# Performance work log

Measured on AMD Instinct MI355X. Metric: run time of the kernel, lower is better.

## Reference

```python
import jax, jax.numpy as jnp
import numpy as np

DIM = 4096
N_HEADS = 32
N_KV_HEADS = 8
HEAD_DIM = 128
ROPE_THETA = 10000.0
REPEATS = N_HEADS // N_KV_HEADS
SCALE = HEAD_DIM ** -0.5


def rope(x, seq_len, offset):
    # x: [b, h, seq_len, head_dim]; faithful to source: cos/sin from cat((freqs,freqs)),
    # rotate built by interleaved pair swap then flatten.
    d = x.shape[-1]
    inv_freq = 1.0 / (ROPE_THETA ** (jnp.arange(0, d, 2, dtype=jnp.float32) / d))  # [d/2]
    t = jnp.arange(offset, offset + seq_len, dtype=jnp.float32)                    # [L]
    freqs = t[:, None] * inv_freq[None, :]                                         # [L, d/2]
    emb = jnp.concatenate([freqs, freqs], axis=-1)                                 # [L, d]
    cos_emb = jnp.cos(emb)
    sin_emb = jnp.sin(emb)
    x_even = x[..., 0::2]
    x_odd = x[..., 1::2]
    rotate_x = jnp.stack([-x_odd, x_even], axis=-1).reshape(x.shape)
    return x * cos_emb + rotate_x * sin_emb


def setup_inputs() -> dict:
    key = jax.random.key(0)
    k1, k2, k3, k4, k5 = jax.random.split(key, 5)
    b, l = 1, 2048
    s = 0.02
    x = jax.random.normal(k1, (b, l, DIM), dtype=jnp.float32)
    wq = jax.random.normal(k2, (DIM, N_HEADS * HEAD_DIM), dtype=jnp.float32) * s
    wk = jax.random.normal(k3, (DIM, N_KV_HEADS * HEAD_DIM), dtype=jnp.float32) * s
    wv = jax.random.normal(k4, (DIM, N_KV_HEADS * HEAD_DIM), dtype=jnp.float32) * s
    wo = jax.random.normal(k5, (N_HEADS * HEAD_DIM, DIM), dtype=jnp.float32) * s
    return {"x": x, "wq": wq, "wk": wk, "wv": wv, "wo": wo, "seq_len": l}


def reference(x, wq, wk, wv, wo, seq_len):
    b, l, _ = x.shape
    q = (x @ wq).reshape(b, l, N_HEADS, HEAD_DIM).transpose(0, 2, 1, 3)       # [b,H,l,d]
    k = (x @ wk).reshape(b, l, N_KV_HEADS, HEAD_DIM).transpose(0, 2, 1, 3)    # [b,Hk,l,d]
    v = (x @ wv).reshape(b, l, N_KV_HEADS, HEAD_DIM).transpose(0, 2, 1, 3)
    # repeat KV heads to match query heads (GQA)
    k = jnp.repeat(k, REPEATS, axis=1)   # [b,H,l,d]
    v = jnp.repeat(v, REPEATS, axis=1)
    offset = 0  # cache is None
    q = rope(q, seq_len, offset)
    k = rope(k, seq_len, offset)
    scores = jnp.einsum('bhid,bhjd->bhij', q * SCALE, k)
    scores = jax.nn.softmax(scores.astype(jnp.float32), axis=-1).astype(scores.dtype)
    out = jnp.einsum('bhij,bhjd->bhid', scores, v)
    out = out.transpose(0, 2, 1, 3).reshape(b, l, N_HEADS * HEAD_DIM)
    return out @ wo, (k, v)
```

## Files before the change

### kernel.cpp

```cpp
#include <hip/hip_runtime.h>
#include <cstdint>
#include <cstddef>

#define DIM 4096
#define SEQ 2048
#define NH 32
#define NKV 8
#define HD 128
#define QKVN 6144

typedef __bf16 bf16_t;
typedef __bf16 bf16x8 __attribute__((ext_vector_type(8)));
typedef __bf16 bf16x4 __attribute__((ext_vector_type(4)));
typedef __bf16 bf16x2 __attribute__((ext_vector_type(2)));
typedef float f32x4 __attribute__((ext_vector_type(4)));
typedef int int4v __attribute__((ext_vector_type(4)));

__device__ __forceinline__ f32x4 mfma16(bf16x8 a, bf16x8 b, f32x4 c) {
  return __builtin_amdgcn_mfma_f32_16x16x32_bf16(a, b, c, 0, 0, 0);
}

__device__ __forceinline__ void async16(const bf16_t* g, bf16_t* l) {
  __builtin_amdgcn_global_load_lds((__attribute__((address_space(1))) void*)g,
                                   (__attribute__((address_space(3))) void*)l,
                                   16, 0, 0);
}

__device__ __forceinline__ int pack2(float a, float b) {
  bf16x2 h = { (bf16_t)a, (bf16_t)b };
  return __builtin_bit_cast(int, h);
}

#define LGKM0() do { asm volatile("s_waitcnt lgkmcnt(0)" ::: "memory"); \
                     __builtin_amdgcn_sched_barrier(0); } while (0)

template <int N> __device__ __forceinline__ void vmw() {
  if constexpr (N == 3) asm volatile("s_waitcnt vmcnt(3)" ::: "memory");
  else if constexpr (N == 4) asm volatile("s_waitcnt vmcnt(4)" ::: "memory");
  else if constexpr (N == 5) asm volatile("s_waitcnt vmcnt(5)" ::: "memory");
  else if constexpr (N == 6) asm volatile("s_waitcnt vmcnt(6)" ::: "memory");
  __builtin_amdgcn_sched_barrier(0);
}

__global__ void cast_x(const float* __restrict__ x, bf16_t* __restrict__ xb) {
  int i = blockIdx.x * 256 + threadIdx.x;
  const float4 v = ((const float4*)x)[i];
  bf16x4 o = { (bf16_t)v.x, (bf16_t)v.y, (bf16_t)v.z, (bf16_t)v.w };
  *(bf16x4*)(xb + (size_t)i * 4) = o;
}

__global__ void tcast(const float* __restrict__ src, bf16_t* __restrict__ dst,
                      int Ncols, int Kdim) {
  __shared__ float tile[32][33];
  int n0 = blockIdx.x * 32, k0 = blockIdx.y * 32;
  int tx = threadIdx.x, ty = threadIdx.y;
#pragma unroll
  for (int r = 0; r < 4; r++)
    tile[ty + 8 * r][tx] = src[(size_t)(k0 + ty + 8 * r) * Ncols + n0 + tx];
  __syncthreads();
#pragma unroll
  for (int r = 0; r < 4; r++)
    dst[(size_t)(n0 + ty + 8 * r) * Kdim + k0 + tx] = (bf16_t)tile[tx][ty + 8 * r];
}

template <int NF>
__global__ __launch_bounds__(512) void gemm256(const bf16_t* __restrict__ A,
                                               const bf16_t* __restrict__ Bt,
                                               float* __restrict__ C,
                                               int M, int N, int K) {
  constexpr int NA = NF - 1;
  constexpr int S1 = 2 + NA;
  __shared__ bf16_t As[2][16384];
  __shared__ bf16_t Bs[2][NF * 4096];
  const int t = threadIdx.x;
  const int lane = t & 63;
  const int l15 = lane & 15, quad = lane >> 4;
  const int w = t >> 6, wm = w >> 2, wn = w & 3;
  const int cgx = l15 & 7;

  const int gx = gridDim.x;
  const int nwg = gx * gridDim.y;
  const int id = blockIdx.y * gx + blockIdx.x;
  const int swz = (id & 7) * (nwg >> 3) + (id >> 3);
  const int bm = (swz / gx) * 256, bn = (swz % gx) * (NF * 64);

  const int srow = t >> 3;
  const int scol = ((t & 7) ^ (srow & 7)) << 3;
  const bf16_t* gA = A + (size_t)(bm + srow) * K + scol;
  const bf16_t* gB = Bt + (size_t)(bn + srow) * K + scol;
  const int ldst = t * 8;

  f32x4 acc[8][NF] = {};
  bf16x8 af[4][2], bfa[NA][2], bfb[2];

  auto sb1 = [&](int b2, int kk) {
    async16(gA + kk, &As[b2][ldst]);
    async16(gA + (size_t)64 * K + kk, &As[b2][4096 + ldst]);
    async16(gB + kk, &Bs[b2][ldst]);
    if constexpr (NF == 3) async16(gB + (size_t)64 * K + kk, &Bs[b2][4096 + ldst]);
  };
  auto sb2 = [&](int b2, int kk) {
    async16(gB + (size_t)((NF - 1) * 64) * K + kk, &Bs[b2][(NF - 1) * 4096 + ldst]);
  };
  auto sb3 = [&](int b2, int kk) {
    async16(gA + (size_t)128 * K + kk, &As[b2][8192 + ldst]);
    async16(gA + (size_t)192 * K + kk, &As[b2][12288 + ldst]);
  };

  sb1(0, 0);
  sb2(0, 0);
  sb3(0, 0);
  vmw<3>();
  __builtin_amdgcn_s_barrier();

  const int nkt = K >> 6;
  for (int kt = 0; kt < nkt; ++kt) {
    const int buf = kt & 1;
    const int k1 = (kt + 1) << 6;
    const bool pf = (kt + 1) < nkt;

#pragma unroll
    for (int mi = 0; mi < 4; mi++)
#pragma unroll
      for (int s = 0; s < 2; s++)
        af[mi][s] = *(const bf16x8*)&As[buf][(wm * 64 + mi * 16 + l15) * 64 +
                                            (((s << 2) | quad) ^ cgx) * 8];
#pragma unroll
    for (int ni = 0; ni < NA; ni++)
#pragma unroll
      for (int s = 0; s < 2; s++)
        bfa[ni][s] = *(const bf16x8*)&Bs[buf][(ni * 64 + wn * 16 + l15) * 64 +
                                              (((s << 2) | quad) ^ cgx) * 8];
    if (pf) sb1(buf ^ 1, k1);
    __builtin_amdgcn_s_barrier();
    LGKM0();
    __builtin_amdgcn_s_setprio(1);
#pragma unroll
    for (int mi = 0; mi < 4; mi++)
#pragma unroll
      for (int ni = 0; ni < NA; ni++)
#pragma unroll
        for (int s = 0; s < 2; s++)
          acc[mi][ni] = mfma16(af[mi][s], bfa[ni][s], acc[mi][ni]);
    __builtin_amdgcn_s_setprio(0);
    vmw<2 + S1>();
    __builtin_amdgcn_s_barrier();

#pragma unroll
    for (int s = 0; s < 2; s++)
      bfb[s] = *(const bf16x8*)&Bs[buf][((NF - 1) * 64 + wn * 16 + l15) * 64 +
                                        (((s << 2) | quad) ^ cgx) * 8];
    if (pf) sb2(buf ^ 1, k1);
    __builtin_amdgcn_s_barrier();
    LGKM0();
    __builtin_amdgcn_s_setprio(1);
#pragma unroll
    for (int mi = 0; mi < 4; mi++)
#pragma unroll
      for (int s = 0; s < 2; s++)
        acc[mi][NF - 1] = mfma16(af[mi][s], bfb[s], acc[mi][NF - 1]);
    __builtin_amdgcn_s_setprio(0);
    vmw<1 + S1>();
    __builtin_amdgcn_s_barrier();

#pragma unroll
    for (int mi = 0; mi < 4; mi++)
#pragma unroll
      for (int s = 0; s < 2; s++)
        af[mi][s] = *(const bf16x8*)&As[buf][(128 + wm * 64 + mi * 16 + l15) * 64 +
                                             (((s << 2) | quad) ^ cgx) * 8];
    if (pf) sb3(buf ^ 1, k1);
    __builtin_amdgcn_s_barrier();
    LGKM0();
    __builtin_amdgcn_s_setprio(1);
#pragma unroll
    for (int mi = 0; mi < 4; mi++)
#pragma unroll
      for (int s = 0; s < 2; s++)
        acc[mi + 4][NF - 1] = mfma16(af[mi][s], bfb[s], acc[mi + 4][NF - 1]);
    __builtin_amdgcn_s_setprio(0);
    __builtin_amdgcn_s_barrier();

#pragma unroll
    for (int ni = 0; ni < NA; ni++)
#pragma unroll
      for (int s = 0; s < 2; s++)
        bfa[ni][s] = *(const bf16x8*)&Bs[buf][(ni * 64 + wn * 16 + l15) * 64 +
                                              (((s << 2) | quad) ^ cgx) * 8];
    __builtin_amdgcn_s_barrier();
    LGKM0();
    __builtin_amdgcn_s_setprio(1);
#pragma unroll
    for (int mi = 0; mi < 4; mi++)
#pragma unroll
      for (int ni = 0; ni < NA; ni++)
#pragma unroll
        for (int s = 0; s < 2; s++)
          acc[mi + 4][ni] = mfma16(af[mi][s], bfa[ni][s], acc[mi + 4][ni]);
    __builtin_amdgcn_s_setprio(0);
    vmw<3>();
    __builtin_amdgcn_s_barrier();
  }

#pragma unroll
  for (int mi = 0; mi < 8; mi++)
#pragma unroll
    for (int ni = 0; ni < NF; ni++) {
      size_t row = (size_t)bm + (mi >> 2) * 128 + wm * 64 + (mi & 3) * 16 + quad * 4;
      size_t col = (size_t)bn + ni * 64 + wn * 16 + l15;
#pragma unroll
      for (int r = 0; r < 4; r++)
        C[(row + r) * N + col] = acc[mi][ni][r];
    }
}

__global__ void rope_scatter(const float* __restrict__ qkv, bf16_t* __restrict__ Qb,
                             bf16_t* __restrict__ Kb, bf16_t* __restrict__ Vt,
                             float* __restrict__ kOut, float* __restrict__ vOut) {
  int idx = blockIdx.x * 256 + threadIdx.x;
  int t = idx / 3072;
  int p = idx - t * 3072;
  const float NEG_L2T_64 = -0.20762050593046f;
  const float SS = 0.08838834764831845f * 1.4426950408889634f;
  if (p < 2048) {
    int hh = p >> 6, pr = p & 63;
    int d0 = pr << 1;
    const float* src = qkv + (size_t)t * QKVN + hh * HD + d0;
    float a = src[0], b = src[1];
    int j0 = d0 & 63, j1 = (d0 + 1) & 63;
    float th0 = (float)t * exp2f((float)j0 * NEG_L2T_64);
    float th1 = (float)t * exp2f((float)j1 * NEG_L2T_64);
    float o0 = (a * cosf(th0) - b * sinf(th0)) * SS;
    float o1 = (b * cosf(th1) + a * sinf(th1)) * SS;
    bf16_t* dst = Qb + ((size_t)hh * SEQ + t) * HD + d0;
    dst[0] = (bf16_t)o0;
    dst[1] = (bf16_t)o1;
  } else if (p < 2560) {
    int q2 = p - 2048;
    int kh = q2 >> 6, pr = q2 & 63;
    int d0 = pr << 1;
    const float* src = qkv + (size_t)t * QKVN + 4096 + kh * HD + d0;
    float a = src[0], b = src[1];
    int j0 = d0 & 63, j1 = (d0 + 1) & 63;
    float th0 = (float)t * exp2f((float)j0 * NEG_L2T_64);
    float th1 = (float)t * exp2f((float)j1 * NEG_L2T_64);
    float o0 = a * cosf(th0) - b * sinf(th0);
    float o1 = b * cosf(th1) + a * sinf(th1);
    bf16_t* dst = Kb + ((size_t)kh * SEQ + t) * HD + d0;
    dst[0] = (bf16_t)o0;
    dst[1] = (bf16_t)o1;
#pragma unroll
    for (int rep = 0; rep < 4; rep++) {
      float* kp = kOut + ((size_t)(kh * 4 + rep) * SEQ + t) * HD + d0;
      kp[0] = o0;
      kp[1] = o1;
    }
  } else {
    int q2 = p - 2560;
    int kh = q2 >> 6, pr = q2 & 63;
    int d0 = pr << 1;
    const float* src = qkv + (size_t)t * QKVN + 5120 + kh * HD + d0;
    float a = src[0], b = src[1];
#pragma unroll
    for (int rep = 0; rep < 4; rep++) {
      float* vp = vOut + ((size_t)(kh * 4 + rep) * SEQ + t) * HD + d0;
      vp[0] = a;
      vp[1] = b;
    }
    int tp = (t & ~31) + ((t & 12) << 1) + (t & 3) + ((t & 16) >> 2);
    Vt[((size_t)kh * HD + d0) * SEQ + tp] = (bf16_t)a;
    Vt[((size_t)kh * HD + d0 + 1) * SEQ + tp] = (bf16_t)b;
  }
}

__global__ __launch_bounds__(512, 2) void attn_kernel(const bf16_t* __restrict__ Qb,
                                                      const bf16_t* __restrict__ Kb,
                                                      const bf16_t* __restrict__ Vt,
                                                      bf16_t* __restrict__ AO) {
  __shared__ bf16_t Ks[2][8192];
  __shared__ bf16_t Vs[2][8192];
  const int h = blockIdx.y, kh = h >> 2;
  const int qbase = blockIdx.x * 256;
  const int w = threadIdx.x >> 6, lane = threadIdx.x & 63;
  const int l15 = lane & 15, quad = lane >> 4;
  const bf16_t* KbH = Kb + (size_t)kh * SEQ * HD;
  const bf16_t* VtH = Vt + (size_t)kh * HD * SEQ;

  bf16x8 qf[2][4];
#pragma unroll
  for (int nq = 0; nq < 2; nq++) {
    const bf16_t* qp = Qb + ((size_t)h * SEQ + qbase + w * 32 + nq * 16 + l15) * HD + quad * 8;
#pragma unroll
    for (int kc = 0; kc < 4; kc++) qf[nq][kc] = *(const bf16x8*)(qp + kc * 32);
  }

  f32x4 acc[8][2] = {};
  float rsum[2] = {0.f, 0.f};

  auto stage = [&](int buf, int kt0) {
    if (w < 4) {
      int kc = w;
#pragma unroll
      for (int kg = 0; kg < 4; kg++) {
        const bf16_t* g = KbH + (size_t)(kt0 + kg * 16 + (lane >> 2)) * HD + kc * 32 + (lane & 3) * 8;
        async16(g, &Ks[buf][kc * 2048 + kg * 512]);
      }
    } else {
      int vi = w - 4, kt = vi >> 1, dg0 = (vi & 1) * 4;
#pragma unroll
      for (int j = 0; j < 4; j++) {
        int dg = dg0 + j;
        const bf16_t* g = VtH + (size_t)(dg * 16 + (lane >> 2)) * SEQ + kt0 + kt * 32 + (lane & 3) * 8;
        async16(g, &Vs[buf][kt * 4096 + dg * 512]);
      }
    }
  };

  stage(0, 0);
  int buf = 0;

  for (int kt0 = 0; kt0 < SEQ; kt0 += 64, buf ^= 1) {
    __syncthreads();
    if (kt0 + 64 < SEQ) stage(buf ^ 1, kt0 + 64);

    f32x4 sacc[4][2] = {};
#pragma unroll
    for (int mi = 0; mi < 4; mi++)
#pragma unroll
      for (int kc = 0; kc < 4; kc++) {
        bf16x8 kf = *(const bf16x8*)(&Ks[buf][(kc * 64 + mi * 16 + l15) * 32 + quad * 8]);
#pragma unroll
        for (int nq = 0; nq < 2; nq++)
          sacc[mi][nq] = mfma16(kf, qf[nq][kc], sacc[mi][nq]);
      }

    int pk[4][2][2];
#pragma unroll
    for (int mi = 0; mi < 4; mi++)
#pragma unroll
      for (int nq = 0; nq < 2; nq++) {
        float p0 = exp2f(sacc[mi][nq][0]);
        float p1 = exp2f(sacc[mi][nq][1]);
        float p2 = exp2f(sacc[mi][nq][2]);
        float p3 = exp2f(sacc[mi][nq][3]);
        rsum[nq] += (p0 + p1) + (p2 + p3);
        pk[mi][nq][0] = pack2(p0, p1);
        pk[mi][nq][1] = pack2(p2, p3);
      }

#pragma unroll
    for (int kt = 0; kt < 2; kt++) {
#pragma unroll
      for (int nq = 0; nq < 2; nq++) {
        int4v dw;
        dw[0] = pk[2 * kt][nq][0];
        dw[1] = pk[2 * kt][nq][1];
        dw[2] = pk[2 * kt + 1][nq][0];
        dw[3] = pk[2 * kt + 1][nq][1];
        bf16x8 pf = __builtin_bit_cast(bf16x8, dw);
#pragma unroll
        for (int dt = 0; dt < 8; dt++) {
          bf16x8 vf = *(const bf16x8*)(&Vs[buf][(kt * 128 + dt * 16 + l15) * 32 + quad * 8]);
          acc[dt][nq] = mfma16(vf, pf, acc[dt][nq]);
        }
      }
    }
  }

#pragma unroll
  for (int nq = 0; nq < 2; nq++) {
    float rs = rsum[nq];
    rs += __shfl_xor(rs, 16);
    rs += __shfl_xor(rs, 32);
    float inv = 1.0f / rs;
    int q = qbase + w * 32 + nq * 16 + l15;
#pragma unroll
    for (int dt = 0; dt < 8; dt++) {
      bf16x4 o = { (bf16_t)(acc[dt][nq][0] * inv), (bf16_t)(acc[dt][nq][1] * inv),
                   (bf16_t)(acc[dt][nq][2] * inv), (bf16_t)(acc[dt][nq][3] * inv) };
      *(bf16x4*)(AO + (size_t)q * DIM + h * HD + dt * 16 + quad * 4) = o;
    }
  }
}

extern "C" void kernel_launch(void* const* d_in, const int* in_sizes, int n_in,
                              void* d_out, int out_size, void* d_ws, size_t ws_size,
                              hipStream_t stream) {
  const float* x = (const float*)d_in[0];
  const float* wq = (const float*)d_in[1];
  const float* wk = (const float*)d_in[2];
  const float* wv = (const float*)d_in[3];
  const float* wo = (const float*)d_in[4];
  float* out = (float*)d_out;
  float* kOut = out + (size_t)SEQ * DIM;
  float* vOut = kOut + (size_t)NH * SEQ * HD;

  char* ws = (char*)d_ws;
  bf16_t* Xb = (bf16_t*)ws;
  bf16_t* WT = (bf16_t*)(ws + 16777216);
  float* QKV = (float*)(ws + 67108864);
  bf16_t* WoT = (bf16_t*)(ws + 67108864);
  bf16_t* Qb = (bf16_t*)(ws + 117440512);
  bf16_t* Kb = (bf16_t*)(ws + 134217728);
  bf16_t* Vt = (bf16_t*)(ws + 138412032);
  bf16_t* AO = Xb;

  dim3 tb(32, 8);
  cast_x<<<8192, 256, 0, stream>>>(x, Xb);
  tcast<<<dim3(128, 128), tb, 0, stream>>>(wq, WT, 4096, 4096);
  tcast<<<dim3(32, 128), tb, 0, stream>>>(wk, WT + (size_t)4096 * 4096, 1024, 4096);
  tcast<<<dim3(32, 128), tb, 0, stream>>>(wv, WT + (size_t)5120 * 4096, 1024, 4096);
  gemm256<3><<<dim3(32, 8), 512, 0, stream>>>(Xb, WT, QKV, 2048, 6144, 4096);
  rope_scatter<<<24576, 256, 0, stream>>>(QKV, Qb, Kb, Vt, kOut, vOut);
  tcast<<<dim3(128, 128), tb, 0, stream>>>(wo, WoT, 4096, 4096);
  attn_kernel<<<dim3(8, 32), 512, 0, stream>>>(Qb, Kb, Vt, AO);
  gemm256<2><<<dim3(32, 8), 512, 0, stream>>>(AO, WoT, out, 2048, 4096, 4096);
}
```

Baseline: 552.1 us.

## Restructure GEMM main loop to prefetch two k-tiles ahead with unrolled double buffer

Reworks the bf16 GEMM k-loop so both LDS buffers are filled up front and each tile's global-to-LDS loads for the tile two steps ahead are issued as one batch. Once all fragments of the current buffer are in registers, that buffer is refilled in place. The loop is unrolled by two so buffer indices are compile-time constants, and the wait counts change to cover a full tile's worth of outstanding loads. The goal is more latency hiding with fewer interleaved partial stages. The cost is extra register pressure from holding both A halves, and the last iterations load wrapped-around (redundant) k data.

```diff
diff --git a/kernel.cpp b/kernel.cpp
--- a/kernel.cpp
+++ b/kernel.cpp
@@ -35,10 +35,8 @@
                      __builtin_amdgcn_sched_barrier(0); } while (0)
 
 template <int N> __device__ __forceinline__ void vmw() {
-  if constexpr (N == 3) asm volatile("s_waitcnt vmcnt(3)" ::: "memory");
-  else if constexpr (N == 4) asm volatile("s_waitcnt vmcnt(4)" ::: "memory");
-  else if constexpr (N == 5) asm volatile("s_waitcnt vmcnt(5)" ::: "memory");
-  else if constexpr (N == 6) asm volatile("s_waitcnt vmcnt(6)" ::: "memory");
+  if constexpr (N == 6) asm volatile("s_waitcnt vmcnt(6)" ::: "memory");
+  else if constexpr (N == 7) asm volatile("s_waitcnt vmcnt(7)" ::: "memory");
   __builtin_amdgcn_sched_barrier(0);
 }
 
@@ -68,8 +66,7 @@
                                                const bf16_t* __restrict__ Bt,
                                                float* __restrict__ C,
                                                int M, int N, int K) {
-  constexpr int NA = NF - 1;
-  constexpr int S1 = 2 + NA;
+  constexpr int NLOAD = 4 + NF;
   __shared__ bf16_t As[2][16384];
   __shared__ bf16_t Bs[2][NF * 4096];
   const int t = threadIdx.x;
@@ -91,115 +88,103 @@
   const int ldst = t * 8;
 
   f32x4 acc[8][NF] = {};
-  bf16x8 af[4][2], bfa[NA][2], bfb[2];
-
-  auto sb1 = [&](int b2, int kk) {
+
+  auto stageT = [&](int b2, int kk) {
     async16(gA + kk, &As[b2][ldst]);
     async16(gA + (size_t)64 * K + kk, &As[b2][4096 + ldst]);
-    async16(gB + kk, &Bs[b2][ldst]);
-    if constexpr (NF == 3) async16(gB + (size_t)64 * K + kk, &Bs[b2][4096 + ldst]);
-  };
-  auto sb2 = [&](int b2, int kk) {
-    async16(gB + (size_t)((NF - 1) * 64) * K + kk, &Bs[b2][(NF - 1) * 4096 + ldst]);
-  };
-  auto sb3 = [&](int b2, int kk) {
     async16(gA + (size_t)128 * K + kk, &As[b2][8192 + ldst]);
     async16(gA + (size_t)192 * K + kk, &As[b2][12288 + ldst]);
+    async16(gB + kk, &Bs[b2][ldst]);
+    async16(gB + (size_t)64 * K + kk, &Bs[b2][4096 + ldst]);
+    if constexpr (NF == 3) async16(gB + (size_t)128 * K + kk, &Bs[b2][8192 + ldst]);
   };
 
-  sb1(0, 0);
-  sb2(0, 0);
-  sb3(0, 0);
-  vmw<3>();
+  stageT(0, 0);
+  stageT(1, 64);
+  vmw<NLOAD>();
   __builtin_amdgcn_s_barrier();
 
-  const int nkt = K >> 6;
-  for (int kt = 0; kt < nkt; ++kt) {
-    const int buf = kt & 1;
-    const int k1 = (kt + 1) << 6;
-    const bool pf = (kt + 1) < nkt;
-
+  auto tile = [&](int b2, int knext) {
+    bf16x8 afl[4][2], afh[4][2], bf01[2][2], bf2[2];
 #pragma unroll
     for (int mi = 0; mi < 4; mi++)
 #pragma unroll
       for (int s = 0; s < 2; s++)
-        af[mi][s] = *(const bf16x8*)&As[buf][(wm * 64 + mi * 16 + l15) * 64 +
-                                            (((s << 2) | quad) ^ cgx) * 8];
-#pragma unroll
-    for (int ni = 0; ni < NA; ni++)
+        afl[mi][s] = *(const bf16x8*)&As[b2][(wm * 64 + mi * 16 + l15) * 64 +
+                                            ((((s << 2) | quad) ^ cgx) << 3)];
+#pragma unroll
+    for (int ni = 0; ni < 2; ni++)
 #pragma unroll
       for (int s = 0; s < 2; s++)
-        bfa[ni][s] = *(const bf16x8*)&Bs[buf][(ni * 64 + wn * 16 + l15) * 64 +
-                                              (((s << 2) | quad) ^ cgx) * 8];
-    if (pf) sb1(buf ^ 1, k1);
+        bf01[ni][s] = *(const bf16x8*)&Bs[b2][(ni * 64 + wn * 16 + l15) * 64 +
+                                              ((((s << 2) | quad) ^ cgx) << 3)];
     __builtin_amdgcn_s_barrier();
     LGKM0();
     __builtin_amdgcn_s_setprio(1);
 #pragma unroll
     for (int mi = 0; mi < 4; mi++)
 #pragma unroll
-      for (int ni = 0; ni < NA; ni++)
+      for (int ni = 0; ni < 2; ni++)
 #pragma unroll
         for (int s = 0; s < 2; s++)
-          acc[mi][ni] = mfma16(af[mi][s], bfa[ni][s], acc[mi][ni]);
-    __builtin_amdgcn_s_setprio(0);
-    vmw<2 + S1>();
-    __builtin_amdgcn_s_barrier();
-
-#pragma unroll
-    for (int s = 0; s < 2; s++)
-      bfb[s] = *(const bf16x8*)&Bs[buf][((NF - 1) * 64 + wn * 16 + l15) * 64 +
-                                        (((s << 2) | quad) ^ cgx) * 8];
-    if (pf) sb2(buf ^ 1, k1);
-    __builtin_amdgcn_s_barrier();
-    LGKM0();
-    __builtin_amdgcn_s_setprio(1);
-#pragma unroll
-    for (int mi = 0; mi < 4; mi++)
-#pragma unroll
-      for (int s = 0; s < 2; s++)
-        acc[mi][NF - 1] = mfma16(af[mi][s], bfb[s], acc[mi][NF - 1]);
-    __builtin_amdgcn_s_setprio(0);
-    vmw<1 + S1>();
-    __builtin_amdgcn_s_barrier();
-
-#pragma unroll
-    for (int mi = 0; mi < 4; mi++)
-#pragma unroll
-      for (int s = 0; s < 2; s++)
-        af[mi][s] = *(const bf16x8*)&As[buf][(128 + wm * 64 + mi * 16 + l15) * 64 +
-                                             (((s << 2) | quad) ^ cgx) * 8];
-    if (pf) sb3(buf ^ 1, k1);
-    __builtin_amdgcn_s_barrier();
-    LGKM0();
-    __builtin_amdgcn_s_setprio(1);
-#pragma unroll
-    for (int mi = 0; mi < 4; mi++)
-#pragma unroll
-      for (int s = 0; s < 2; s++)
-        acc[mi + 4][NF - 1] = mfma16(af[mi][s], bfb[s], acc[mi + 4][NF - 1]);
+          acc[mi][ni] = mfma16(afl[mi][s], bf01[ni][s], acc[mi][ni]);
     __builtin_amdgcn_s_setprio(0);
     __builtin_amdgcn_s_barrier();
 
 #pragma unroll
-    for (int ni = 0; ni < NA; ni++)
+    for (int mi = 0; mi < 4; mi++)
 #pragma unroll
       for (int s = 0; s < 2; s++)
-        bfa[ni][s] = *(const bf16x8*)&Bs[buf][(ni * 64 + wn * 16 + l15) * 64 +
-                                              (((s << 2) | quad) ^ cgx) * 8];
+        afh[mi][s] = *(const bf16x8*)&As[b2][(128 + wm * 64 + mi * 16 + l15) * 64 +
+                                             ((((s << 2) | quad) ^ cgx) << 3)];
+    if constexpr (NF == 2) {
+      LGKM0();
+      __builtin_amdgcn_s_barrier();
+      stageT(b2, knext);
+      __builtin_amdgcn_sched_barrier(0);
+    } else {
+      __builtin_amdgcn_s_barrier();
+      LGKM0();
+    }
+    __builtin_amdgcn_s_setprio(1);
+#pragma unroll
+    for (int mi = 0; mi < 4; mi++)
+#pragma unroll
+      for (int ni = 0; ni < 2; ni++)
+#pragma unroll
+        for (int s = 0; s < 2; s++)
+          acc[mi + 4][ni] = mfma16(afh[mi][s], bf01[ni][s], acc[mi + 4][ni]);
+    __builtin_amdgcn_s_setprio(0);
+    if constexpr (NF == 2) vmw<NLOAD>();
     __builtin_amdgcn_s_barrier();
-    LGKM0();
-    __builtin_amdgcn_s_setprio(1);
-#pragma unroll
-    for (int mi = 0; mi < 4; mi++)
-#pragma unroll
-      for (int ni = 0; ni < NA; ni++)
-#pragma unroll
-        for (int s = 0; s < 2; s++)
-          acc[mi + 4][ni] = mfma16(af[mi][s], bfa[ni][s], acc[mi + 4][ni]);
-    __builtin_amdgcn_s_setprio(0);
-    vmw<3>();
-    __builtin_amdgcn_s_barrier();
+
+    if constexpr (NF == 3) {
+#pragma unroll
+      for (int s = 0; s < 2; s++)
+        bf2[s] = *(const bf16x8*)&Bs[b2][(128 + wn * 16 + l15) * 64 +
+                                         ((((s << 2) | quad) ^ cgx) << 3)];
+      LGKM0();
+      __builtin_amdgcn_s_barrier();
+      stageT(b2, knext);
+      __builtin_amdgcn_sched_barrier(0);
+      __builtin_amdgcn_s_setprio(1);
+#pragma unroll
+      for (int mi = 0; mi < 4; mi++)
+#pragma unroll
+        for (int s = 0; s < 2; s++) {
+          acc[mi][2] = mfma16(afl[mi][s], bf2[s], acc[mi][2]);
+          acc[mi + 4][2] = mfma16(afh[mi][s], bf2[s], acc[mi + 4][2]);
+        }
+      __builtin_amdgcn_s_setprio(0);
+      vmw<NLOAD>();
+      __builtin_amdgcn_s_barrier();
+    }
+  };
+
+  const int nit = K >> 7;
+  for (int i = 0; i < nit; ++i) {
+    tile(0, ((i << 7) + 128) & (K - 1));
+    tile(1, ((i << 7) + 192) & (K - 1));
   }
 
 #pragma unroll
```

Measured after the change: 537.8 us. -2.6%, faster.
